# Kernel tuning notes

Hardware: AMD Instinct MI355X
Metric: run time of the kernel (lower is better)

The kernel has to match this reference:

```python
import jax, jax.numpy as jnp
import numpy as np

HIDDEN = 768
HEADS = 8
EXP = 4
EPS = 1e-5


def layer_norm(x, g, b):
    mu = jnp.mean(x, axis=-1, keepdims=True)
    var = jnp.mean(jnp.square(x - mu), axis=-1, keepdims=True)
    return (x - mu) * jax.lax.rsqrt(var + EPS) * g + b


def setup_inputs() -> dict:
    key = jax.random.key(0)
    ks = jax.random.split(key, 16)
    h, e = HIDDEN, EXP * HIDDEN
    s = 0.02
    return {
        "x": jax.random.normal(ks[0], (2, 4096, h), dtype=jnp.float32),
        "ln1_g": jnp.ones((h,), jnp.float32),
        "ln1_b": jnp.zeros((h,), jnp.float32),
        "wq": jax.random.normal(ks[1], (h, h), jnp.float32) * s,
        "bq": jnp.zeros((h,), jnp.float32),
        "wk": jax.random.normal(ks[2], (h, h), jnp.float32) * s,
        "bk": jnp.zeros((h,), jnp.float32),
        "wv": jax.random.normal(ks[3], (h, h), jnp.float32) * s,
        "bv": jnp.zeros((h,), jnp.float32),
        "wp": jax.random.normal(ks[4], (h, h), jnp.float32) * s,
        "bp": jnp.zeros((h,), jnp.float32),
        "ln2_g": jnp.ones((h,), jnp.float32),
        "ln2_b": jnp.zeros((h,), jnp.float32),
        "w1": jax.random.normal(ks[5], (h, e), jnp.float32) * s,
        "b1": jnp.zeros((e,), jnp.float32),
        "w2": jax.random.normal(ks[6], (e, h), jnp.float32) * s,
        "b2": jnp.zeros((h,), jnp.float32),
    }


def reference(x, ln1_g, ln1_b, wq, bq, wk, bk, wv, bv, wp, bp,
              ln2_g, ln2_b, w1, b1, w2, b2):
    n, s, h = x.shape
    d = h // HEADS

    # --- MSA branch (pre-LN) ---
    xn = layer_norm(x, ln1_g, ln1_b)
    q = (xn @ wq + bq).reshape(n, s, HEADS, d).transpose(0, 2, 1, 3)  # bhsd
    k = (xn @ wk + bk).reshape(n, s, HEADS, d).transpose(0, 2, 1, 3)
    v = (xn @ wv + bv).reshape(n, s, HEADS, d).transpose(0, 2, 1, 3)
    energy = jnp.einsum('bhqd,bhkd->bhqk', q, k)
    # faithful to original: softmax over the HEAD axis (dim=1), then scale
    att = jax.nn.softmax(energy, axis=1) / (h ** 0.5)
    attn_out = jnp.einsum('bhqk,bhkd->bhqd', att, v)
    attn_out = attn_out.transpose(0, 2, 1, 3).reshape(n, s, h)
    attn_out = attn_out @ wp + bp
    x = x + attn_out

    # --- MLP branch (pre-LN) ---
    xn = layer_norm(x, ln2_g, ln2_b)
    hmid = jax.nn.gelu(xn @ w1 + b1, approximate=False)
    x = x + (hmid @ w2 + b2)
    return x
```

## Files before the change

kernel.cpp:

```cpp
#include <hip/hip_runtime.h>
#include <cstdint>
#include <cstddef>

#define AS1 __attribute__((address_space(1)))
#define AS3 __attribute__((address_space(3)))

typedef __attribute__((ext_vector_type(8))) __bf16 bf16x8;
typedef __attribute__((ext_vector_type(4))) float f32x4;

__device__ __forceinline__ void gload_lds16(const void* g, void* l) {
  __builtin_amdgcn_global_load_lds((AS1 void*)g, (AS3 void*)l, 16, 0, 0);
}

__global__ void k_transpose_w(const float* __restrict__ src, __bf16* __restrict__ dst,
                              int K, int N, int ldd, int koff) {
  __shared__ float tile[32][33];
  const int bx = blockIdx.x * 32;
  const int by = blockIdx.y * 32;
  const int tx = threadIdx.x, ty = threadIdx.y;
#pragma unroll
  for (int ii = 0; ii < 4; ++ii) {
    int i = ty + ii * 8;
    tile[i][tx] = src[(size_t)(by + i) * N + bx + tx];
  }
  __syncthreads();
#pragma unroll
  for (int ii = 0; ii < 4; ++ii) {
    int i = ty + ii * 8;
    dst[(size_t)(bx + i) * ldd + koff + by + tx] = (__bf16)tile[tx][i];
  }
}

__global__ void k_pack_bias(const float* __restrict__ bq, const float* __restrict__ bk,
                            const float* __restrict__ bv, float* __restrict__ dst) {
  int i = blockIdx.x * 256 + threadIdx.x;
  if (i < 768) dst[i] = bq[i];
  else if (i < 1536) dst[i] = bk[i - 768];
  else if (i < 2304) dst[i] = bv[i - 1536];
}

__global__ __launch_bounds__(256) void k_layernorm(const float* __restrict__ x,
                                                   const float* __restrict__ g,
                                                   const float* __restrict__ b,
                                                   __bf16* __restrict__ out) {
  const int row = blockIdx.x * 4 + (threadIdx.x >> 6);
  const int lane = threadIdx.x & 63;
  const float* xr = x + (size_t)row * 768;
  float4 v[3];
#pragma unroll
  for (int j = 0; j < 3; ++j) v[j] = *(const float4*)(xr + j * 256 + lane * 4);
  float s = 0.f, ss = 0.f;
#pragma unroll
  for (int j = 0; j < 3; ++j) {
    s += v[j].x + v[j].y + v[j].z + v[j].w;
    ss += v[j].x * v[j].x + v[j].y * v[j].y + v[j].z * v[j].z + v[j].w * v[j].w;
  }
#pragma unroll
  for (int off = 32; off > 0; off >>= 1) {
    s += __shfl_xor(s, off);
    ss += __shfl_xor(ss, off);
  }
  const float mu = s * (1.f / 768.f);
  const float rstd = rsqrtf(ss * (1.f / 768.f) - mu * mu + 1e-5f);
  __bf16* orow = out + (size_t)row * 768;
#pragma unroll
  for (int j = 0; j < 3; ++j) {
    float4 gg = *(const float4*)(g + j * 256 + lane * 4);
    float4 bb = *(const float4*)(b + j * 256 + lane * 4);
    const int base = j * 256 + lane * 4;
    orow[base + 0] = (__bf16)((v[j].x - mu) * rstd * gg.x + bb.x);
    orow[base + 1] = (__bf16)((v[j].y - mu) * rstd * gg.y + bb.y);
    orow[base + 2] = (__bf16)((v[j].z - mu) * rstd * gg.z + bb.z);
    orow[base + 3] = (__bf16)((v[j].w - mu) * rstd * gg.w + bb.w);
  }
}

template <int MODE>
__global__ __launch_bounds__(256) void k_gemm(const __bf16* __restrict__ A,
                                              const __bf16* __restrict__ BT,
                                              const float* __restrict__ bias,
                                              const float* __restrict__ resid,
                                              void* __restrict__ Cout,
                                              int M, int N, int K) {
  __shared__ __bf16 As[128 * 32];
  __shared__ __bf16 Bs[128 * 32];
  const int m0 = blockIdx.y * 128, n0 = blockIdx.x * 128;
  const int tid = threadIdx.x;
  const int wid = tid >> 6, lane = tid & 63;
  const int wm = wid >> 1, wn = wid & 1;
  const int lr = lane & 15, lg = lane >> 4;

  f32x4 acc[4][4] = {};

  for (int k0 = 0; k0 < K; k0 += 32) {
#pragma unroll
    for (int it = 0; it < 2; ++it) {
      int t = tid + it * 256;
      int r = t >> 2, c = (t & 3) * 8;
      gload_lds16(A + (size_t)(m0 + r) * K + k0 + c, As + t * 8);
      gload_lds16(BT + (size_t)(n0 + r) * K + k0 + c, Bs + t * 8);
    }
    __syncthreads();
    bf16x8 af[4], bf[4];
#pragma unroll
    for (int i = 0; i < 4; ++i) af[i] = *(const bf16x8*)(As + (wm * 64 + i * 16 + lr) * 32 + lg * 8);
#pragma unroll
    for (int j = 0; j < 4; ++j) bf[j] = *(const bf16x8*)(Bs + (wn * 64 + j * 16 + lr) * 32 + lg * 8);
#pragma unroll
    for (int i = 0; i < 4; ++i)
#pragma unroll
      for (int j = 0; j < 4; ++j)
        acc[i][j] = __builtin_amdgcn_mfma_f32_16x16x32_bf16(af[i], bf[j], acc[i][j], 0, 0, 0);
    __syncthreads();
  }

#pragma unroll
  for (int i = 0; i < 4; ++i)
#pragma unroll
    for (int j = 0; j < 4; ++j)
#pragma unroll
      for (int r = 0; r < 4; ++r) {
        int row = m0 + wm * 64 + i * 16 + lg * 4 + r;
        int col = n0 + wn * 64 + j * 16 + lr;
        float v = acc[i][j][r] + bias[col];
        size_t idx = (size_t)row * N + col;
        if constexpr (MODE == 0) {
          if (col < 768) v *= 1.44269504088896f;
          ((__bf16*)Cout)[idx] = (__bf16)v;
        } else if constexpr (MODE == 1) {
          ((float*)Cout)[idx] = v + resid[idx];
        } else {
          float u = 0.7978845608f * (v + 0.044715f * v * v * v);
          float t = __builtin_amdgcn_exp2f(u * 2.88539008f);
          float th = 1.f - 2.f * __builtin_amdgcn_rcpf(t + 1.f);
          ((__bf16*)Cout)[idx] = (__bf16)(0.5f * v * (1.f + th));
        }
      }
}

__global__ __launch_bounds__(256) void k_pack_ka(const __bf16* __restrict__ qkv,
                                                 __bf16* __restrict__ KA) {
  const int kb = blockIdx.x, b = blockIdx.y;
  const int t = threadIdx.x;
#pragma unroll
  for (int i = 0; i < 6; ++i) {
    int c = t + i * 256;
    int lane = c & 63, f = c >> 6;
    int dc = f % 3, hh = (f / 3) & 1, hp = f / 6;
    int row = kb * 16 + (lane & 15);
    int col = 768 + hp * 192 + hh * 96 + dc * 32 + (lane >> 4) * 8;
    bf16x8 v = *(const bf16x8*)(qkv + (size_t)(b * 4096 + row) * 2304 + col);
    *(bf16x8*)(KA + ((size_t)(b * 256 + kb) * 1536 + c) * 8) = v;
  }
}

__global__ __launch_bounds__(256) void k_pack_va(const __bf16* __restrict__ qkv,
                                                 __bf16* __restrict__ VA) {
  __shared__ __bf16 vtile[32][772];
  const int g = blockIdx.x, b = blockIdx.y;
  const int t = threadIdx.x;
#pragma unroll
  for (int i = 0; i < 12; ++i) {
    int c = t + i * 256;
    int row = c / 96, c8 = c % 96;
    *(bf16x8*)(&vtile[row][c8 * 8]) =
        *(const bf16x8*)(qkv + (size_t)(b * 4096 + g * 32 + row) * 2304 + 1536 + c8 * 8);
  }
  __syncthreads();
#pragma unroll
  for (int i = 0; i < 12; ++i) {
    int c = t + i * 256;
    int lane = c & 63, f = c >> 6;
    int db = f % 6, hh = (f / 6) & 1, hp = f / 12;
    int d = hp * 192 + hh * 96 + db * 16 + (lane & 15);
    int lg_ = lane >> 4;
    bf16x8 v;
#pragma unroll
    for (int e = 0; e < 8; ++e) {
      int krow = (e >> 2) * 16 + lg_ * 4 + (e & 3);
      v[e] = vtile[krow][d];
    }
    *(bf16x8*)(VA + ((size_t)(b * 128 + g) * 3072 + c) * 8) = v;
  }
}

__global__ __launch_bounds__(1024, 4) void k_attn(const __bf16* __restrict__ qkv,
                                                  const __bf16* __restrict__ KA,
                                                  const __bf16* __restrict__ VA,
                                                  __bf16* __restrict__ attn4) {
  __shared__ __bf16 Kb_s[2][12288];
  __shared__ __bf16 Vb_s[24576];
  __shared__ float ps_s[2][4352];
  const int bid = blockIdx.x;
  const int slice = bid & 7;
  const int b = slice >> 2, ks = slice & 3;
  const int qb = bid >> 3;
  const int wid = threadIdx.x >> 6;
  const int qs = wid & 3, hp = wid >> 2;
  const int q0 = qb * 64 + qs * 16;
  const int lane = threadIdx.x & 63;
  const int lr = lane & 15, lg = lane >> 4;

  const __bf16* Qb = qkv + (size_t)(b * 4096 + q0) * 2304;
  bf16x8 qf[2][3];
#pragma unroll
  for (int hh = 0; hh < 2; ++hh)
#pragma unroll
    for (int dc = 0; dc < 3; ++dc)
      qf[hh][dc] = *(const bf16x8*)(Qb + (size_t)lr * 2304 + (hp * 2 + hh) * 96 + dc * 32 + lg * 8);

  const int L1 = wid, hpK1 = L1 / 6, jK1 = L1 - hpK1 * 6;
  const int L2 = wid + 16, hpK2 = L2 / 6, jK2 = L2 - hpK2 * 6;

  int kb = ks * 64;
  {
    const __bf16* srcK = KA + (size_t)(b * 256 + kb) * 12288;
    gload_lds16(srcK + hpK1 * 3072 + jK1 * 512 + lane * 8,
                &Kb_s[0][hpK1 * 3072 + jK1 * 512 + lane * 8]);
    if (wid < 8)
      gload_lds16(srcK + hpK2 * 3072 + jK2 * 512 + lane * 8,
                  &Kb_s[0][hpK2 * 3072 + jK2 * 512 + lane * 8]);
  }
  asm volatile("s_waitcnt vmcnt(0)" ::: "memory");
  __builtin_amdgcn_s_barrier();
  asm volatile("" ::: "memory");

  f32x4 o[2][6] = {};
  f32x4 eA[2], eB[2];

#define HALF(ET, PAR, DO_V, DO_PV) do {                                               \
    {                      \
      size_t kidx = (size_t)(b * 256 + kb + 1);                                       \
      if (kidx > 511) kidx = 511;                                                     \
      const __bf16* srcK = KA + kidx * 12288;                                         \
      gload_lds16(srcK + hpK1 * 3072 + jK1 * 512 + lane * 8,                          \
                  &Kb_s[PAR ^ 1][hpK1 * 3072 + jK1 * 512 + lane * 8]);                \
      if (wid < 8)                                                                    \
        gload_lds16(srcK + hpK2 * 3072 + jK2 * 512 + lane * 8,                        \
                    &Kb_s[PAR ^ 1][hpK2 * 3072 + jK2 * 512 + lane * 8]);              \
    }                                                                                 \
    if (DO_V) {     \
      const __bf16* srcV = VA + (size_t)(b * 128 + (kb >> 1)) * 24576;                \
      _Pragma("unroll")                                                               \
      for (int tt = 0; tt < 3; ++tt) {                                                \
        int L = wid * 3 + tt;                                                         \
        int hpV = L / 12, jV = L - hpV * 12;                                          \
        gload_lds16(srcV + hpV * 6144 + jV * 512 + lane * 8,                          \
                    &Vb_s[hpV * 6144 + jV * 512 + lane * 8]);                         \
      }                                                                               \
    }                                                                                 \
                                                                   \
    ET[0] = (f32x4){0.f, 0.f, 0.f, 0.f};                                              \
    ET[1] = (f32x4){0.f, 0.f, 0.f, 0.f};                                              \
    {                                                                                 \
      const __bf16* kbase = &Kb_s[PAR][hp * 3072 + lane * 8];                         \
      __builtin_amdgcn_s_setprio(1);                                                  \
      _Pragma("unroll")                                                               \
      for (int hh = 0; hh < 2; ++hh)                                                  \
        _Pragma("unroll")                                                             \
        for (int dc = 0; dc < 3; ++dc) {                                              \
          bf16x8 kf = *(const bf16x8*)(kbase + (hh * 3 + dc) * 512);                  \
          ET[hh] = __builtin_amdgcn_mfma_f32_16x16x32_bf16(kf, qf[hh][dc], ET[hh],    \
                                                           0, 0, 0);                  \
        }                                                                             \
      __builtin_amdgcn_s_setprio(0);                                                  \
    }                                                                                 \
              \
    _Pragma("unroll")                                                                 \
    for (int rr = 0; rr < 4; ++rr) {                                                  \
      float e0 = __builtin_amdgcn_exp2f(ET[0][rr]);                                   \
      float e1 = __builtin_amdgcn_exp2f(ET[1][rr]);                                   \
      ET[0][rr] = e0;                                                                 \
      ET[1][rr] = e1;                                                                 \
      ps_s[PAR][qs * 1088 + (lg * 4 + rr) * 68 + hp * 17 + lr] = e0 + e1;             \
    }                                                                                 \
    if (DO_V) {                                                                       \
      asm volatile("s_waitcnt vmcnt(3) lgkmcnt(0)" ::: "memory");                     \
    } else {                                                                          \
      asm volatile("s_waitcnt vmcnt(0) lgkmcnt(0)" ::: "memory");                     \
    }                                                                                 \
    __builtin_amdgcn_s_barrier();                                                     \
    asm volatile("" ::: "memory");                                                    \
                                    \
    {                                                                                 \
      float inv_[4];                                                                  \
      _Pragma("unroll")                                                               \
      for (int rr = 0; rr < 4; ++rr) {                                                \
        const int base = qs * 1088 + (lg * 4 + rr) * 68 + lr;                         \
        float tot = (ps_s[PAR][base] + ps_s[PAR][base + 17]) +                        \
                    (ps_s[PAR][base + 34] + ps_s[PAR][base + 51]);                    \
        inv_[rr] = 0.03608439182435161f * __builtin_amdgcn_rcpf(tot);                 \
      }                                                                               \
      _Pragma("unroll")                                                               \
      for (int rr = 0; rr < 4; ++rr) {                                                \
        ET[0][rr] *= inv_[rr];                                                        \
        ET[1][rr] *= inv_[rr];                                                        \
      }                                                                               \
    }                                                                                 \
    if (DO_PV) {            \
      bf16x8 pf0, pf1;                                                                \
      _Pragma("unroll")                                                               \
      for (int e2 = 0; e2 < 8; ++e2) {                                                \
        int rr = e2 & 3;                                                              \
        if (e2 < 4) { pf0[e2] = (__bf16)eA[0][rr]; pf1[e2] = (__bf16)eA[1][rr]; }     \
        else        { pf0[e2] = (__bf16)eB[0][rr]; pf1[e2] = (__bf16)eB[1][rr]; }     \
      }                                                                               \
      const __bf16* vbase = &Vb_s[hp * 6144 + lane * 8];                              \
      __builtin_amdgcn_s_setprio(1);                                                  \
      _Pragma("unroll")                                                               \
      for (int db = 0; db < 6; ++db) {                                                \
        bf16x8 vf0 = *(const bf16x8*)(vbase + db * 512);                              \
        bf16x8 vf1 = *(const bf16x8*)(vbase + (6 + db) * 512);                        \
        o[0][db] = __builtin_amdgcn_mfma_f32_16x16x32_bf16(pf0, vf0, o[0][db], 0, 0, 0); \
        o[1][db] = __builtin_amdgcn_mfma_f32_16x16x32_bf16(pf1, vf1, o[1][db], 0, 0, 0); \
      }                                                                               \
      __builtin_amdgcn_s_setprio(0);                                                  \
    }                                                                                 \
    ++kb;                                                                             \
  } while (0)

  for (int rp = 0; rp < 64; rp += 2) {
    HALF(eA, 0, 1, 0);
    HALF(eB, 1, 0, 1);
  }
#undef HALF

#pragma unroll
  for (int hh = 0; hh < 2; ++hh)
#pragma unroll
    for (int db = 0; db < 6; ++db)
#pragma unroll
      for (int rr = 0; rr < 4; ++rr)
        attn4[(size_t)(b * 4096 + q0 + lg * 4 + rr) * 3072 + ks * 768 +
              (hp * 2 + hh) * 96 + db * 16 + lr] = (__bf16)o[hh][db][rr];
}

__global__ __launch_bounds__(256) void k_reduce_attn(const __bf16* __restrict__ attn4,
                                                     __bf16* __restrict__ out) {
  int g = blockIdx.x * 256 + threadIdx.x;
  int row = g / 96, c8 = g % 96;
  const __bf16* p = attn4 + (size_t)row * 3072 + c8 * 8;
  float acc[8] = {};
#pragma unroll
  for (int s = 0; s < 4; ++s) {
    bf16x8 v = *(const bf16x8*)(p + s * 768);
#pragma unroll
    for (int e = 0; e < 8; ++e) acc[e] += (float)v[e];
  }
  bf16x8 r;
#pragma unroll
  for (int e = 0; e < 8; ++e) r[e] = (__bf16)acc[e];
  *(bf16x8*)(out + (size_t)row * 768 + c8 * 8) = r;
}

extern "C" void kernel_launch(void* const* d_in, const int* in_sizes, int n_in,
                              void* d_out, int out_size, void* d_ws, size_t ws_size,
                              hipStream_t stream) {
  (void)in_sizes; (void)n_in; (void)out_size; (void)ws_size;
  const float* x     = (const float*)d_in[0];
  const float* ln1_g = (const float*)d_in[1];
  const float* ln1_b = (const float*)d_in[2];
  const float* wq    = (const float*)d_in[3];
  const float* bq    = (const float*)d_in[4];
  const float* wk    = (const float*)d_in[5];
  const float* bk    = (const float*)d_in[6];
  const float* wv    = (const float*)d_in[7];
  const float* bv    = (const float*)d_in[8];
  const float* wp    = (const float*)d_in[9];
  const float* bp    = (const float*)d_in[10];
  const float* ln2_g = (const float*)d_in[11];
  const float* ln2_b = (const float*)d_in[12];
  const float* w1    = (const float*)d_in[13];
  const float* b1    = (const float*)d_in[14];
  const float* w2    = (const float*)d_in[15];
  const float* b2    = (const float*)d_in[16];

  char* ws = (char*)d_ws;
  const size_t o_wqkvT = 0;
  const size_t o_wpT   = o_wqkvT + (size_t)2304 * 768 * 2;
  const size_t o_w1T   = o_wpT   + (size_t)768 * 768 * 2;
  const size_t o_w2T   = o_w1T   + (size_t)768 * 3072 * 2;
  const size_t o_bqkv  = o_w2T   + (size_t)3072 * 768 * 2;
  const size_t o_xn    = o_bqkv  + (size_t)2304 * 4;
  const size_t o_qkv   = o_xn    + (size_t)8192 * 768 * 2;
  const size_t o_KA    = o_qkv   + (size_t)8192 * 2304 * 2;
  const size_t o_VA    = o_KA    + (size_t)2 * 256 * 1536 * 8 * 2;
  const size_t o_attn4 = o_VA    + (size_t)2 * 128 * 3072 * 8 * 2;
  const size_t o_x1      = o_attn4;
  const size_t o_attnred = o_KA;
  const size_t o_xn2     = o_VA;
  const size_t o_hmid    = o_xn;

  __bf16* wqkvT = (__bf16*)(ws + o_wqkvT);
  __bf16* wpT   = (__bf16*)(ws + o_wpT);
  __bf16* w1T   = (__bf16*)(ws + o_w1T);
  __bf16* w2T   = (__bf16*)(ws + o_w2T);
  float*  bqkv  = (float*)(ws + o_bqkv);
  __bf16* xn    = (__bf16*)(ws + o_xn);
  __bf16* qkvb  = (__bf16*)(ws + o_qkv);
  __bf16* KA    = (__bf16*)(ws + o_KA);
  __bf16* VA    = (__bf16*)(ws + o_VA);
  __bf16* attn4 = (__bf16*)(ws + o_attn4);
  float*  x1    = (float*)(ws + o_x1);
  __bf16* attnr = (__bf16*)(ws + o_attnred);
  __bf16* xn2   = (__bf16*)(ws + o_xn2);
  __bf16* hmid  = (__bf16*)(ws + o_hmid);

  dim3 tb(32, 8);
  k_transpose_w<<<dim3(24, 24), tb, 0, stream>>>(wq, wqkvT, 768, 768, 768, 0);
  k_transpose_w<<<dim3(24, 24), tb, 0, stream>>>(wk, wqkvT + (size_t)768 * 768, 768, 768, 768, 0);
  k_transpose_w<<<dim3(24, 24), tb, 0, stream>>>(wv, wqkvT + (size_t)2 * 768 * 768, 768, 768, 768, 0);
  k_transpose_w<<<dim3(24, 24), tb, 0, stream>>>(wp, wpT, 768, 768, 768, 0);
  k_transpose_w<<<dim3(96, 24), tb, 0, stream>>>(w1, w1T, 768, 3072, 768, 0);
  k_transpose_w<<<dim3(24, 96), tb, 0, stream>>>(w2, w2T, 3072, 768, 3072, 0);
  k_pack_bias<<<9, 256, 0, stream>>>(bq, bk, bv, bqkv);

  k_layernorm<<<2048, 256, 0, stream>>>(x, ln1_g, ln1_b, xn);
  k_gemm<0><<<dim3(18, 64), 256, 0, stream>>>(xn, wqkvT, bqkv, nullptr, qkvb, 8192, 2304, 768);
  k_pack_ka<<<dim3(256, 2), 256, 0, stream>>>(qkvb, KA);
  k_pack_va<<<dim3(128, 2), 256, 0, stream>>>(qkvb, VA);
  k_attn<<<512, 1024, 0, stream>>>(qkvb, KA, VA, attn4);
  k_reduce_attn<<<3072, 256, 0, stream>>>(attn4, attnr);
  k_gemm<1><<<dim3(6, 64), 256, 0, stream>>>(attnr, wpT, bp, x, x1, 8192, 768, 768);
  k_layernorm<<<2048, 256, 0, stream>>>(x1, ln2_g, ln2_b, xn2);
  k_gemm<2><<<dim3(24, 64), 256, 0, stream>>>(xn2, w1T, b1, nullptr, hmid, 8192, 3072, 768);
  k_gemm<1><<<dim3(6, 64), 256, 0, stream>>>(hmid, w2T, b2, x1, (float*)d_out, 8192, 768, 3072);
}
```

Measured before the change: 497.4 us.

## Remap GEMM blocks per XCD and split-K the MLP down-projection

Flattens the GEMM grid to 1D and remaps block indices so that consecutive blocks on each XCD (blockIdx mod 8) cover contiguous row bands, which is meant to improve L2 reuse of A tiles. It also splits the K=3072 down-projection GEMM into two K=1536 halves that write bf16 partial products, then adds a small fused kernel that sums the partials with bias and residual. This doubles the block count for the under-occupied 384-block GEMM. The cost is extra global traffic for the partials and an extra launch, and the bf16 rounding of the partials costs some precision.

Result: faster. 469.9 us (-5.5%).

```diff
diff --git a/kernel.cpp b/kernel.cpp
--- a/kernel.cpp
+++ b/kernel.cpp
@@ -81,10 +81,19 @@
                                               const float* __restrict__ bias,
                                               const float* __restrict__ resid,
                                               void* __restrict__ Cout,
-                                              int M, int N, int K) {
+                                              int M, int N, int K, int lda, int ldb) {
   __shared__ __bf16 As[128 * 32];
   __shared__ __bf16 Bs[128 * 32];
-  const int m0 = blockIdx.y * 128, n0 = blockIdx.x * 128;
+  const int nx = N >> 7;
+  const int rpx = (M >> 7) >> 3;
+  const int xcd = blockIdx.x & 7;
+  const int ib = blockIdx.x >> 3;
+  const int n0 = (ib % nx) << 7;
+  const int m0 = (xcd * rpx + ib / nx) << 7;
+  if constexpr (MODE == 3) {
+    A += (size_t)blockIdx.y * K;
+    BT += (size_t)blockIdx.y * K;
+  }
   const int tid = threadIdx.x;
   const int wid = tid >> 6, lane = tid & 63;
   const int wm = wid >> 1, wn = wid & 1;
@@ -97,8 +106,8 @@
     for (int it = 0; it < 2; ++it) {
       int t = tid + it * 256;
       int r = t >> 2, c = (t & 3) * 8;
-      gload_lds16(A + (size_t)(m0 + r) * K + k0 + c, As + t * 8);
-      gload_lds16(BT + (size_t)(n0 + r) * K + k0 + c, Bs + t * 8);
+      gload_lds16(A + (size_t)(m0 + r) * lda + k0 + c, As + t * 8);
+      gload_lds16(BT + (size_t)(n0 + r) * ldb + k0 + c, Bs + t * 8);
     }
     __syncthreads();
     bf16x8 af[4], bf[4];
@@ -122,20 +131,50 @@
       for (int r = 0; r < 4; ++r) {
         int row = m0 + wm * 64 + i * 16 + lg * 4 + r;
         int col = n0 + wn * 64 + j * 16 + lr;
-        float v = acc[i][j][r] + bias[col];
+        float v = acc[i][j][r];
+        if constexpr (MODE != 3) v += bias[col];
         size_t idx = (size_t)row * N + col;
         if constexpr (MODE == 0) {
           if (col < 768) v *= 1.44269504088896f;
           ((__bf16*)Cout)[idx] = (__bf16)v;
         } else if constexpr (MODE == 1) {
           ((float*)Cout)[idx] = v + resid[idx];
-        } else {
+        } else if constexpr (MODE == 2) {
           float u = 0.7978845608f * (v + 0.044715f * v * v * v);
           float t = __builtin_amdgcn_exp2f(u * 2.88539008f);
           float th = 1.f - 2.f * __builtin_amdgcn_rcpf(t + 1.f);
           ((__bf16*)Cout)[idx] = (__bf16)(0.5f * v * (1.f + th));
+        } else {
+          ((__bf16*)Cout)[(size_t)blockIdx.y * M * N + idx] = (__bf16)v;
         }
       }
+}
+
+__global__ __launch_bounds__(256) void k_fuse_mlp2(const __bf16* __restrict__ p0,
+                                                   const __bf16* __restrict__ p1,
+                                                   const float* __restrict__ bias,
+                                                   const float* __restrict__ resid,
+                                                   float* __restrict__ out) {
+  int g = blockIdx.x * 256 + threadIdx.x;
+  int base = g * 8;
+  int col = base % 768;
+  bf16x8 a = *(const bf16x8*)(p0 + base);
+  bf16x8 b = *(const bf16x8*)(p1 + base);
+  float4 r0 = *(const float4*)(resid + base);
+  float4 r1 = *(const float4*)(resid + base + 4);
+  float4 b0 = *(const float4*)(bias + col);
+  float4 b1 = *(const float4*)(bias + col + 4);
+  float4 o0, o1;
+  o0.x = r0.x + b0.x + (float)a[0] + (float)b[0];
+  o0.y = r0.y + b0.y + (float)a[1] + (float)b[1];
+  o0.z = r0.z + b0.z + (float)a[2] + (float)b[2];
+  o0.w = r0.w + b0.w + (float)a[3] + (float)b[3];
+  o1.x = r1.x + b1.x + (float)a[4] + (float)b[4];
+  o1.y = r1.y + b1.y + (float)a[5] + (float)b[5];
+  o1.z = r1.z + b1.z + (float)a[6] + (float)b[6];
+  o1.w = r1.w + b1.w + (float)a[7] + (float)b[7];
+  *(float4*)(out + base) = o0;
+  *(float4*)(out + base + 4) = o1;
 }
 
 __global__ __launch_bounds__(256) void k_pack_ka(const __bf16* __restrict__ qkv,
@@ -387,6 +426,7 @@
   const size_t o_VA    = o_KA    + (size_t)2 * 256 * 1536 * 8 * 2;
   const size_t o_attn4 = o_VA    + (size_t)2 * 128 * 3072 * 8 * 2;
   const size_t o_x1      = o_attn4;
+  const size_t o_part    = o_attn4 + (size_t)8192 * 768 * 4;
   const size_t o_attnred = o_KA;
   const size_t o_xn2     = o_VA;
   const size_t o_hmid    = o_xn;
@@ -402,6 +442,7 @@
   __bf16* VA    = (__bf16*)(ws + o_VA);
   __bf16* attn4 = (__bf16*)(ws + o_attn4);
   float*  x1    = (float*)(ws + o_x1);
+  __bf16* part  = (__bf16*)(ws + o_part);
   __bf16* attnr = (__bf16*)(ws + o_attnred);
   __bf16* xn2   = (__bf16*)(ws + o_xn2);
   __bf16* hmid  = (__bf16*)(ws + o_hmid);
@@ -416,13 +457,16 @@
   k_pack_bias<<<9, 256, 0, stream>>>(bq, bk, bv, bqkv);
 
   k_layernorm<<<2048, 256, 0, stream>>>(x, ln1_g, ln1_b, xn);
-  k_gemm<0><<<dim3(18, 64), 256, 0, stream>>>(xn, wqkvT, bqkv, nullptr, qkvb, 8192, 2304, 768);
+  k_gemm<0><<<1152, 256, 0, stream>>>(xn, wqkvT, bqkv, nullptr, qkvb, 8192, 2304, 768, 768, 768);
   k_pack_ka<<<dim3(256, 2), 256, 0, stream>>>(qkvb, KA);
   k_pack_va<<<dim3(128, 2), 256, 0, stream>>>(qkvb, VA);
   k_attn<<<512, 1024, 0, stream>>>(qkvb, KA, VA, attn4);
   k_reduce_attn<<<3072, 256, 0, stream>>>(attn4, attnr);
-  k_gemm<1><<<dim3(6, 64), 256, 0, stream>>>(attnr, wpT, bp, x, x1, 8192, 768, 768);
+  k_gemm<1><<<384, 256, 0, stream>>>(attnr, wpT, bp, x, x1, 8192, 768, 768, 768, 768);
   k_layernorm<<<2048, 256, 0, stream>>>(x1, ln2_g, ln2_b, xn2);
-  k_gemm<2><<<dim3(24, 64), 256, 0, stream>>>(xn2, w1T, b1, nullptr, hmid, 8192, 3072, 768);
-  k_gemm<1><<<dim3(6, 64), 256, 0, stream>>>(hmid, w2T, b2, x1, (float*)d_out, 8192, 768, 3072);
-}
+  k_gemm<2><<<1536, 256, 0, stream>>>(xn2, w1T, b1, nullptr, hmid, 8192, 3072, 768, 768, 768);
+  k_gemm<3><<<dim3(384, 2), 256, 0, stream>>>(hmid, w2T, nullptr, nullptr, part,
+                                              8192, 768, 1536, 3072, 3072);
+  k_fuse_mlp2<<<3072, 256, 0, stream>>>(part, part + (size_t)8192 * 768, b2, x1,
+                                        (float*)d_out);
+}
```
